# Performance work log

Measured on AMD Instinct MI355X. Metric: run time of the kernel, lower is better.

The kernel has to match this reference:

```python
import jax, jax.numpy as jnp
import numpy as np

N, D, P, H = 4096, 128, 128, 256  # n samples, input_dim, pe_dim, hidden_dim


def setup_inputs() -> dict:
    key = jax.random.key(0)
    k0, k1, k2 = jax.random.split(key, 3)
    x = jax.random.normal(k0, (N, D), dtype=jnp.float32)
    # shared_net params: Linear(D+P -> H), Linear(H -> 1)
    W1 = jax.random.normal(k1, (D + P, H), dtype=jnp.float32) / np.sqrt(D + P).astype(np.float32)
    b1 = jnp.zeros((H,), dtype=jnp.float32)
    W2 = jax.random.normal(k2, (H, 1), dtype=jnp.float32) / np.sqrt(H).astype(np.float32)
    b2 = jnp.zeros((1,), dtype=jnp.float32)
    return {"x": x, "W1": W1, "b1": b1, "W2": W2, "b2": b2}


def reference(x, W1, b1, W2, b2):
    """Vectorized NIMO.forward: all d feature-masked MLP evals in one batched GEMM.

    Original python loop: for each j, zero column j of x, append one-hot pe[:, :P],
    run shared MLP -> g_j (n,), column j of B is x[:, j] * (1 + g_j).
    Output B has shape (n, d+1) with a leading ones column.
    Dropout(noise_std=0.0) is identity.
    """
    n, d = x.shape
    p = W1.shape[0] - d
    dt = x.dtype
    # (d, n, d): x replicated d times with column j zeroed in slice j
    mask = (1.0 - jnp.eye(d)).astype(dt)
    x_masked = x[None, :, :] * mask[:, None, :]
    # First linear layer, split into masked-x part and (constant per j) pe part.
    h = jnp.einsum('jni,ih->jnh', x_masked, W1[:d])          # (d, n, h)
    pe_add = jnp.eye(d, dtype=dt)[:, :p] @ W1[d:]            # (d, h): one-hot pe through W1
    h = jax.nn.relu(h + pe_add[:, None, :] + b1)
    g = jnp.einsum('jnh,ho->jno', h, W2)[..., 0] + b2[0]     # (d, n)
    cols = x * (1.0 + g.T)                                   # (n, d)
    return jnp.concatenate([jnp.ones((n, 1), dtype=dt), cols], axis=1)  # (n, d+1)
```

## Files before the change

kernel.cpp:

```cpp
#include <hip/hip_runtime.h>


#define NROWS 4096
#define DIN   128
#define HDIM  256
#define JCH   16

__global__ __launch_bounds__(256) void nimo_base(
    const float* __restrict__ x, const float* __restrict__ W1,
    const float* __restrict__ b1, float* __restrict__ baseb)
{
    __shared__ float xs[DIN * 36];
    const int tid  = threadIdx.x;
    const int row0 = blockIdx.x * 32;
    const int h0   = blockIdx.y * 64;

    {
        const int bidx = tid * 16;
        const int r = bidx >> 7;
        const int c = bidx & 127;
        #pragma unroll
        for (int u = 0; u < 4; ++u) {
            const float4 v = *(const float4*)(x + (size_t)(row0 + r) * DIN + c + u * 4);
            xs[(c + u * 4 + 0) * 36 + r] = v.x;
            xs[(c + u * 4 + 1) * 36 + r] = v.y;
            xs[(c + u * 4 + 2) * 36 + r] = v.z;
            xs[(c + u * 4 + 3) * 36 + r] = v.w;
        }
    }
    __syncthreads();

    const int tx = tid & 31;
    const int ty = tid >> 5;
    const float* __restrict__ wcol = W1 + h0 + tx * 2;

    float2 acc[4];
    #pragma unroll
    for (int u = 0; u < 4; ++u) { acc[u].x = 0.f; acc[u].y = 0.f; }

    #pragma unroll 8
    for (int k = 0; k < DIN; ++k) {
        const float2 w  = *(const float2*)(wcol + (size_t)k * HDIM);
        const float4 xv = *(const float4*)(&xs[k * 36 + ty * 4]);
        acc[0].x = fmaf(xv.x, w.x, acc[0].x); acc[0].y = fmaf(xv.x, w.y, acc[0].y);
        acc[1].x = fmaf(xv.y, w.x, acc[1].x); acc[1].y = fmaf(xv.y, w.y, acc[1].y);
        acc[2].x = fmaf(xv.z, w.x, acc[2].x); acc[2].y = fmaf(xv.z, w.y, acc[2].y);
        acc[3].x = fmaf(xv.w, w.x, acc[3].x); acc[3].y = fmaf(xv.w, w.y, acc[3].y);
    }

    const float2 bv = *(const float2*)(b1 + h0 + tx * 2);
    #pragma unroll
    for (int u = 0; u < 4; ++u) {
        float2 o; o.x = acc[u].x + bv.x; o.y = acc[u].y + bv.y;
        *(float2*)(baseb + (size_t)(row0 + ty * 4 + u) * HDIM + h0 + tx * 2) = o;
    }
}

__global__ __launch_bounds__(512, 4) void nimo_main(
    const float* __restrict__ x, const float* __restrict__ W1,
    const float* __restrict__ W2, const float* __restrict__ b2,
    const float* __restrict__ baseb, float* __restrict__ out)
{
    __shared__ float part[8][JCH][64];
    const int tid  = threadIdx.x;
    const int r    = tid & 63;
    const int q    = tid >> 6;
    const int row0 = blockIdx.x * 64;
    const int row  = row0 + r;
    const int j0   = blockIdx.y * JCH;
    const int h0   = __builtin_amdgcn_readfirstlane(q * 32);

    float bb[32];
    {
        const float4* bp = (const float4*)(baseb + (size_t)row * HDIM + h0);
        #pragma unroll
        for (int u = 0; u < 8; ++u) ((float4*)bb)[u] = bp[u];
    }
    float w2r[32];
    {
        const float* __restrict__ w2p = W2 + h0;
        #pragma unroll
        for (int u = 0; u < 32; ++u) w2r[u] = w2p[u];
    }

    const float* __restrict__ xrow = x + (size_t)row * DIN;
    float nxj = xrow[j0];

    for (int jj = 0; jj < JCH; ++jj) {
        const float xj = nxj;
        if (jj + 1 < JCH) nxj = xrow[j0 + jj + 1];
        const float* __restrict__ wa = W1 + (size_t)(j0 + jj) * HDIM + h0;
        const float* __restrict__ wp = wa + DIN * HDIM;
        float acc = 0.f;
        #pragma unroll
        for (int h = 0; h < 32; ++h) {
            float t = bb[h] + wp[h];
            t = fmaf(-xj, wa[h], t);
            t = fmaxf(t, 0.f);
            acc = fmaf(t, w2r[h], acc);
        }
        part[q][jj][r] = acc;
    }
    __syncthreads();

    const float b2s = b2[0];
    if (blockIdx.y == 0 && tid < 64) out[(size_t)(row0 + tid) * 129] = 1.0f;

    #pragma unroll
    for (int e = 0; e < 2; ++e) {
        const int idx = e * 512 + tid;
        const int jj  = idx >> 6;
        const int rr  = idx & 63;
        float g = 0.f;
        #pragma unroll
        for (int qq = 0; qq < 8; ++qq) g += part[qq][jj][rr];
        const float xv = x[(size_t)(row0 + rr) * DIN + j0 + jj];
        out[(size_t)(row0 + rr) * 129 + 1 + j0 + jj] = xv * (1.0f + g + b2s);
    }
}

extern "C" void kernel_launch(void* const* d_in, const int* in_sizes, int n_in,
                              void* d_out, int out_size, void* d_ws, size_t ws_size,
                              hipStream_t stream) {
    const float* x  = (const float*)d_in[0];
    const float* W1 = (const float*)d_in[1];
    const float* b1 = (const float*)d_in[2];
    const float* W2 = (const float*)d_in[3];
    const float* b2 = (const float*)d_in[4];
    float* out = (float*)d_out;
    float* baseb = (float*)d_ws;

    nimo_base<<<dim3(NROWS / 32, HDIM / 64), 256, 0, stream>>>(x, W1, b1, baseb);
    nimo_main<<<dim3(NROWS / 64, DIN / JCH), 512, 0, stream>>>(x, W1, W2, b2, baseb, out);
}
```

Baseline: 93.47 us.

## Stage W1 and x slices in shared memory and halve j-chunk per block

Result: slower. 149.3 us (+59.7%).

```diff
diff --git a/kernel.cpp b/kernel.cpp
--- a/kernel.cpp
+++ b/kernel.cpp
@@ -4,7 +4,7 @@
 #define NROWS 4096
 #define DIN   128
 #define HDIM  256
-#define JCH   16
+#define JCH   8
 
 __global__ __launch_bounds__(256) void nimo_base(
     const float* __restrict__ x, const float* __restrict__ W1,
@@ -61,43 +61,52 @@
     const float* __restrict__ W2, const float* __restrict__ b2,
     const float* __restrict__ baseb, float* __restrict__ out)
 {
-    __shared__ float part[8][JCH][64];
+    __shared__ float sa[JCH][HDIM];
+    __shared__ float sp[JCH][HDIM];
+    __shared__ float xs[64][JCH + 1];
+    __shared__ float part[8][JCH][66];
+
     const int tid  = threadIdx.x;
     const int r    = tid & 63;
     const int q    = tid >> 6;
     const int row0 = blockIdx.x * 64;
     const int row  = row0 + r;
     const int j0   = blockIdx.y * JCH;
-    const int h0   = __builtin_amdgcn_readfirstlane(q * 32);
+    const int h0   = q * 32;
 
-    float bb[32];
+    {
+        const float4* wsrc = (const float4*)(W1 + (size_t)j0 * HDIM);
+        const float4* psrc = (const float4*)(W1 + (size_t)(DIN + j0) * HDIM);
+        ((float4*)&sa[0][0])[tid] = wsrc[tid];
+        ((float4*)&sp[0][0])[tid] = psrc[tid];
+        const int xr = tid >> 3;
+        const int xc = tid & 7;
+        xs[xr][xc] = x[(size_t)(row0 + xr) * DIN + j0 + xc];
+    }
+
+    float bb[32], w2r[32];
     {
         const float4* bp = (const float4*)(baseb + (size_t)row * HDIM + h0);
+        const float4* wp2 = (const float4*)(W2 + h0);
         #pragma unroll
-        for (int u = 0; u < 8; ++u) ((float4*)bb)[u] = bp[u];
+        for (int u = 0; u < 8; ++u) { ((float4*)bb)[u] = bp[u]; ((float4*)w2r)[u] = wp2[u]; }
     }
-    float w2r[32];
-    {
-        const float* __restrict__ w2p = W2 + h0;
-        #pragma unroll
-        for (int u = 0; u < 32; ++u) w2r[u] = w2p[u];
-    }
-
-    const float* __restrict__ xrow = x + (size_t)row * DIN;
-    float nxj = xrow[j0];
+    __syncthreads();
 
     for (int jj = 0; jj < JCH; ++jj) {
-        const float xj = nxj;
-        if (jj + 1 < JCH) nxj = xrow[j0 + jj + 1];
-        const float* __restrict__ wa = W1 + (size_t)(j0 + jj) * HDIM + h0;
-        const float* __restrict__ wp = wa + DIN * HDIM;
+        const float xj = xs[r][jj];
+        const float* wa = &sa[jj][h0];
+        const float* wp = &sp[jj][h0];
         float acc = 0.f;
         #pragma unroll
-        for (int h = 0; h < 32; ++h) {
-            float t = bb[h] + wp[h];
-            t = fmaf(-xj, wa[h], t);
-            t = fmaxf(t, 0.f);
-            acc = fmaf(t, w2r[h], acc);
+        for (int u = 0; u < 8; ++u) {
+            const float4 a4 = *(const float4*)(wa + u * 4);
+            const float4 p4 = *(const float4*)(wp + u * 4);
+            float t;
+            t = fmaf(-xj, a4.x, bb[u*4+0] + p4.x); t = fmaxf(t, 0.f); acc = fmaf(t, w2r[u*4+0], acc);
+            t = fmaf(-xj, a4.y, bb[u*4+1] + p4.y); t = fmaxf(t, 0.f); acc = fmaf(t, w2r[u*4+1], acc);
+            t = fmaf(-xj, a4.z, bb[u*4+2] + p4.z); t = fmaxf(t, 0.f); acc = fmaf(t, w2r[u*4+2], acc);
+            t = fmaf(-xj, a4.w, bb[u*4+3] + p4.w); t = fmaxf(t, 0.f); acc = fmaf(t, w2r[u*4+3], acc);
         }
         part[q][jj][r] = acc;
     }
@@ -106,15 +115,13 @@
     const float b2s = b2[0];
     if (blockIdx.y == 0 && tid < 64) out[(size_t)(row0 + tid) * 129] = 1.0f;
 
-    #pragma unroll
-    for (int e = 0; e < 2; ++e) {
-        const int idx = e * 512 + tid;
-        const int jj  = idx >> 6;
-        const int rr  = idx & 63;
+    {
+        const int rr = tid >> 3;
+        const int jj = tid & 7;
         float g = 0.f;
         #pragma unroll
         for (int qq = 0; qq < 8; ++qq) g += part[qq][jj][rr];
-        const float xv = x[(size_t)(row0 + rr) * DIN + j0 + jj];
+        const float xv = xs[rr][jj];
         out[(size_t)(row0 + rr) * 129 + 1 + j0 + jj] = xv * (1.0f + g + b2s);
     }
 }
```
